# Performance work log

Hardware: AMD Instinct MI355X
Metric: run time of the kernel (lower is better)

The kernel has to match this reference:

```python
import jax, jax.numpy as jnp
import numpy as np

B, S = 16, 1024
V, D, P = 100000, 256, 8


def setup_inputs() -> dict:
    key = jax.random.key(0)
    k1, k2, k3, k4 = jax.random.split(key, 4)
    x = jax.random.randint(k1, (B, S), 0, V, dtype=jnp.int64 if jax.config.jax_enable_x64 else jnp.int32)
    emb_table = jax.random.normal(k2, (V, D), dtype=jnp.float32)
    weight = jax.random.normal(k3, (P, D, D), dtype=jnp.float32)
    partitions = jax.random.randint(k4, (V,), 0, P, dtype=jnp.int32)
    return {"x": x, "emb_table": emb_table, "weight": weight, "partitions": partitions}


def reference(x, emb_table, weight, partitions):
    P_, Dz, Dx = weight.shape
    # mask[p, x] = 1 for x < D >> p (reset_parameters halves active dim per partition)
    active = (Dx >> jnp.arange(P_))  # [P]
    mask = (jnp.arange(Dx)[None, :] < active[:, None]).astype(weight.dtype)  # [P, Dx]
    mw = weight * mask[:, None, :]  # [P, Dz, Dx], masked partition weights

    emb = emb_table[x]          # [B, S, Dx] token embeddings
    part = partitions[x]        # [B, S] partition id per token

    # Compute all P candidate outputs (small fixed P), then select per token.
    # Mathematically identical to gathering mw[part] and doing per-token matvec,
    # but avoids the huge [B,S,Dz,Dx] gathered-weight intermediate.
    all_out = jnp.einsum('bsx,pzx->bspz', emb, mw)  # [B, S, P, Dz]
    out = jnp.take_along_axis(all_out, part[..., None, None], axis=2)[..., 0, :]  # [B, S, Dz]
    return out
```

## Files before the change

### kernel.cpp

```cpp
#include <hip/hip_runtime.h>

__global__ void bucket_k(const int* __restrict__ x, const int* __restrict__ parts,
                         int* __restrict__ counts, int* __restrict__ buckets, int NT) {
    __shared__ int lcount[8];
    __shared__ int lbase[8];
    const int tid = threadIdx.x;
    if (tid < 8) lcount[tid] = 0;
    __syncthreads();

    const int i = blockIdx.x * blockDim.x + tid;
    int p = 0, lpos = 0;
    const bool valid = (i < NT);
    if (valid) {
        p = parts[x[i]];
        lpos = atomicAdd(&lcount[p], 1);
    }
    __syncthreads();
    if (tid < 8)
        lbase[tid] = lcount[tid] ? atomicAdd(&counts[tid], lcount[tid]) : 0;
    __syncthreads();
    if (valid)
        buckets[(size_t)p * NT + lbase[p] + lpos] = i;
}

#define TT 32
#define KC 32
#define XB 80

__global__ __launch_bounds__(256)
void fge_gemm(const int* __restrict__ x,
              const float* __restrict__ emb,
              const float* __restrict__ weight,
              const int* __restrict__ counts,
              const int* __restrict__ buckets,
              float* __restrict__ out, int NT) {
    const int p = blockIdx.y;
    const int n = counts[p];
    if ((int)(blockIdx.x * TT) >= n) return;
    const int K   = 256 >> p;
    const int nch = (K + KC - 1) / KC;
    const int tid = threadIdx.x;

    __shared__ __align__(16) float e_lds[KC][TT];
    __shared__ __align__(16) float w_lds[KC][256];
    __shared__ int vrow[TT];
    __shared__ int oidx[TT];

    const int tt  = tid & 7;
    const int tz  = tid >> 3;
    const int t_s = tid & 31;
    const int xh  = tid >> 5;

    for (int t0 = blockIdx.x * TT; t0 < n; t0 += XB * TT) {
        const int ntile = min(TT, n - t0);

        __syncthreads();
        if (tid < TT) {
            int idx = 0, row = 0;
            if (tid < ntile) {
                idx = buckets[(size_t)p * NT + t0 + tid];
                row = x[idx];
            }
            oidx[tid] = idx;
            vrow[tid] = row;
        }
        __syncthreads();

        float acc[4][8] = {};

        for (int ch = 0; ch < nch; ++ch) {
            {
                const bool tv = (t_s < ntile);
                const int gxb = ch * KC + xh * 4;
                const float4 v = *(const float4*)(emb + (size_t)vrow[t_s] * 256 + gxb);
                const float va[4] = {v.x, v.y, v.z, v.w};
#pragma unroll
                for (int c = 0; c < 4; ++c)
                    e_lds[xh * 4 + c][t_s] = (tv && (gxb + c) < K) ? va[c] : 0.f;
            }
            {
                const float* wr = weight + ((size_t)p * 256 + tid) * 256 + ch * KC;
#pragma unroll
                for (int i = 0; i < KC / 4; ++i) {
                    const float4 v = *(const float4*)(wr + i * 4);
                    w_lds[i * 4 + 0][tid] = v.x;
                    w_lds[i * 4 + 1][tid] = v.y;
                    w_lds[i * 4 + 2][tid] = v.z;
                    w_lds[i * 4 + 3][tid] = v.w;
                }
            }
            __syncthreads();

#pragma unroll
            for (int c = 0; c < KC; ++c) {
                const float4 ev = *(const float4*)&e_lds[c][tt * 4];
                const float4 w0 = *(const float4*)&w_lds[c][tz * 8];
                const float4 w1 = *(const float4*)&w_lds[c][tz * 8 + 4];
                const float ea[4] = {ev.x, ev.y, ev.z, ev.w};
                const float wa[8] = {w0.x, w0.y, w0.z, w0.w, w1.x, w1.y, w1.z, w1.w};
#pragma unroll
                for (int i = 0; i < 4; ++i)
#pragma unroll
                    for (int j = 0; j < 8; ++j)
                        acc[i][j] = fmaf(ea[i], wa[j], acc[i][j]);
            }
            __syncthreads();
        }

#pragma unroll
        for (int i = 0; i < 4; ++i) {
            const int t = tt * 4 + i;
            if (t < ntile) {
                float* op = out + (size_t)oidx[t] * 256 + tz * 8;
                float4 o0 = {acc[i][0], acc[i][1], acc[i][2], acc[i][3]};
                float4 o1 = {acc[i][4], acc[i][5], acc[i][6], acc[i][7]};
                *(float4*)op = o0;
                *(float4*)(op + 4) = o1;
            }
        }
    }
}

__global__ void naive_k(const int* __restrict__ x, const float* __restrict__ emb,
                        const float* __restrict__ w, const int* __restrict__ parts,
                        float* __restrict__ out, int D, int P) {
    const int i = blockIdx.x;
    const int tokrow = x[i];
    const int p = parts[tokrow];
    const int K = D >> p;
    const float* er = emb + (size_t)tokrow * D;
    for (int z = threadIdx.x; z < D; z += blockDim.x) {
        const float* wr = w + ((size_t)p * D + z) * D;
        float acc = 0.f;
        for (int k = 0; k < K; ++k) acc = fmaf(er[k], wr[k], acc);
        out[(size_t)i * D + z] = acc;
    }
}

extern "C" void kernel_launch(void* const* d_in, const int* in_sizes, int n_in,
                              void* d_out, int out_size, void* d_ws, size_t ws_size,
                              hipStream_t stream) {
    const int*   xi    = (const int*)d_in[0];
    const float* emb   = (const float*)d_in[1];
    const float* wgt   = (const float*)d_in[2];
    const int*   parts = (const int*)d_in[3];
    float* out = (float*)d_out;

    const int NT = in_sizes[0];
    const long long V = in_sizes[3];
    const int D = (int)(in_sizes[1] / V);
    const int P = (int)(in_sizes[2] / ((long long)D * D));
    const size_t need = 32 + (size_t)P * (size_t)NT * sizeof(int);

    if (D == 256 && P == 8 && ws_size >= need) {
        int* counts  = (int*)d_ws;
        int* buckets = (int*)((char*)d_ws + 32);
        hipMemsetAsync(counts, 0, 32, stream);
        bucket_k<<<(NT + 255) / 256, 256, 0, stream>>>(xi, parts, counts, buckets, NT);
        dim3 grid(XB, 8);
        fge_gemm<<<grid, 256, 0, stream>>>(xi, emb, wgt, counts, buckets, out, NT);
    } else {
        naive_k<<<NT, 256, 0, stream>>>(xi, emb, wgt, parts, out, D, P);
    }
}
```

Baseline: 170.0 us.

## Retile bucketed GEMM into 64-token by 64-output tiles with swizzled LDS

Reorganizes the per-partition GEMM to split the output dimension across 4 blocks (a new grid z dimension for partitions) with 64-token tiles. Each thread now computes 4 tokens by 4 outputs. The K chunk adapts to the partition's active width, up to 64, with a minimum of 16, so small partitions waste less padding. Weight LDS is stored transposed with an XOR-like rotation to avoid bank conflicts. The aim is more parallel blocks, better coalesced embedding loads and less wasted work on masked K, at the cost of re-gathering embeddings for each of the 4 z-blocks.

```diff
diff --git a/kernel.cpp b/kernel.cpp
--- a/kernel.cpp
+++ b/kernel.cpp
@@ -23,9 +23,8 @@
         buckets[(size_t)p * NT + lbase[p] + lpos] = i;
 }
 
-#define TT 32
-#define KC 32
-#define XB 80
+#define TT 64
+#define XB 40
 
 __global__ __launch_bounds__(256)
 void fge_gemm(const int* __restrict__ x,
@@ -34,22 +33,23 @@
               const int* __restrict__ counts,
               const int* __restrict__ buckets,
               float* __restrict__ out, int NT) {
-    const int p = blockIdx.y;
+    const int p = blockIdx.z;
     const int n = counts[p];
     if ((int)(blockIdx.x * TT) >= n) return;
+    const int z0  = blockIdx.y * 64;
     const int K   = 256 >> p;
-    const int nch = (K + KC - 1) / KC;
+    const int KP  = (K < 16) ? 16 : K;
+    const int KC  = (KP < 64) ? KP : 64;
+    const int nch = KP / KC;
     const int tid = threadIdx.x;
 
-    __shared__ __align__(16) float e_lds[KC][TT];
-    __shared__ __align__(16) float w_lds[KC][256];
+    __shared__ __align__(16) float e_lds[TT * 64];
+    __shared__ __align__(16) float w_lds[64 * 64];
     __shared__ int vrow[TT];
     __shared__ int oidx[TT];
 
-    const int tt  = tid & 7;
-    const int tz  = tid >> 3;
-    const int t_s = tid & 31;
-    const int xh  = tid >> 5;
+    const int tg  = tid >> 4;
+    const int zg4 = (tid & 15) * 4;
 
     for (int t0 = blockIdx.x * TT; t0 < n; t0 += XB * TT) {
         const int ntile = min(TT, n - t0);
@@ -66,56 +66,82 @@
         }
         __syncthreads();
 
-        float acc[4][8] = {};
+        float acc[4][4] = {};
 
         for (int ch = 0; ch < nch; ++ch) {
+            const int kbase = ch * KC;
+            const int lpr   = KC >> 2;
+
             {
-                const bool tv = (t_s < ntile);
-                const int gxb = ch * KC + xh * 4;
-                const float4 v = *(const float4*)(emb + (size_t)vrow[t_s] * 256 + gxb);
-                const float va[4] = {v.x, v.y, v.z, v.w};
-#pragma unroll
-                for (int c = 0; c < 4; ++c)
-                    e_lds[xh * 4 + c][t_s] = (tv && (gxb + c) < K) ? va[c] : 0.f;
+                const int passes = (TT * lpr) >> 8;
+                for (int ps = 0; ps < passes; ++ps) {
+                    const int idx = ps * 256 + tid;
+                    const int row = idx / lpr;
+                    const int c4  = (idx - row * lpr) * 4;
+                    const float4 v = *(const float4*)(emb + (size_t)vrow[row] * 256 + kbase + c4);
+                    float4 o;
+                    o.x = (kbase + c4 + 0 < K) ? v.x : 0.f;
+                    o.y = (kbase + c4 + 1 < K) ? v.y : 0.f;
+                    o.z = (kbase + c4 + 2 < K) ? v.z : 0.f;
+                    o.w = (kbase + c4 + 3 < K) ? v.w : 0.f;
+                    *(float4*)&e_lds[row * KC + c4] = o;
+                }
             }
             {
-                const float* wr = weight + ((size_t)p * 256 + tid) * 256 + ch * KC;
+                const int passes = (64 * lpr) >> 8;
+                for (int ps = 0; ps < passes; ++ps) {
+                    const int idx = ps * 256 + tid;
+                    const int rz  = idx / lpr;
+                    const int c4  = (idx - rz * lpr) * 4;
+                    const float4 v = *(const float4*)(weight + ((size_t)p * 256 + z0 + rz) * 256 + kbase + c4);
+                    const float vv[4] = {v.x, v.y, v.z, v.w};
 #pragma unroll
-                for (int i = 0; i < KC / 4; ++i) {
-                    const float4 v = *(const float4*)(wr + i * 4);
-                    w_lds[i * 4 + 0][tid] = v.x;
-                    w_lds[i * 4 + 1][tid] = v.y;
-                    w_lds[i * 4 + 2][tid] = v.z;
-                    w_lds[i * 4 + 3][tid] = v.w;
+                    for (int j = 0; j < 4; ++j) {
+                        const int kk = c4 + j;
+                        w_lds[kk * 64 + ((rz + 4 * kk) & 63)] =
+                            (kbase + kk < K) ? vv[j] : 0.f;
+                    }
                 }
             }
             __syncthreads();
 
+            const float* e0 = &e_lds[(tg * 4 + 0) * KC];
+            const float* e1 = &e_lds[(tg * 4 + 1) * KC];
+            const float* e2 = &e_lds[(tg * 4 + 2) * KC];
+            const float* e3 = &e_lds[(tg * 4 + 3) * KC];
+#pragma unroll 2
+            for (int k = 0; k < KC; k += 4) {
+                const float4 a0 = *(const float4*)(e0 + k);
+                const float4 a1 = *(const float4*)(e1 + k);
+                const float4 a2 = *(const float4*)(e2 + k);
+                const float4 a3 = *(const float4*)(e3 + k);
+                float4 w[4];
 #pragma unroll
-            for (int c = 0; c < KC; ++c) {
-                const float4 ev = *(const float4*)&e_lds[c][tt * 4];
-                const float4 w0 = *(const float4*)&w_lds[c][tz * 8];
-                const float4 w1 = *(const float4*)&w_lds[c][tz * 8 + 4];
-                const float ea[4] = {ev.x, ev.y, ev.z, ev.w};
-                const float wa[8] = {w0.x, w0.y, w0.z, w0.w, w1.x, w1.y, w1.z, w1.w};
+                for (int j = 0; j < 4; ++j)
+                    w[j] = *(const float4*)&w_lds[(k + j) * 64 + ((zg4 + 4 * (k + j)) & 63)];
+                const float ea[4][4] = {{a0.x,a0.y,a0.z,a0.w}, {a1.x,a1.y,a1.z,a1.w},
+                                        {a2.x,a2.y,a2.z,a2.w}, {a3.x,a3.y,a3.z,a3.w}};
+                const float wv[4][4] = {{w[0].x,w[0].y,w[0].z,w[0].w}, {w[1].x,w[1].y,w[1].z,w[1].w},
+                                        {w[2].x,w[2].y,w[2].z,w[2].w}, {w[3].x,w[3].y,w[3].z,w[3].w}};
 #pragma unroll
                 for (int i = 0; i < 4; ++i)
 #pragma unroll
-                    for (int j = 0; j < 8; ++j)
-                        acc[i][j] = fmaf(ea[i], wa[j], acc[i][j]);
+                    for (int j = 0; j < 4; ++j) {
+                        acc[i][0] = fmaf(ea[i][j], wv[j][0], acc[i][0]);
+                        acc[i][1] = fmaf(ea[i][j], wv[j][1], acc[i][1]);
+                        acc[i][2] = fmaf(ea[i][j], wv[j][2], acc[i][2]);
+                        acc[i][3] = fmaf(ea[i][j], wv[j][3], acc[i][3]);
+                    }
             }
             __syncthreads();
         }
 
 #pragma unroll
         for (int i = 0; i < 4; ++i) {
-            const int t = tt * 4 + i;
+            const int t = tg * 4 + i;
             if (t < ntile) {
-                float* op = out + (size_t)oidx[t] * 256 + tz * 8;
-                float4 o0 = {acc[i][0], acc[i][1], acc[i][2], acc[i][3]};
-                float4 o1 = {acc[i][4], acc[i][5], acc[i][6], acc[i][7]};
-                *(float4*)op = o0;
-                *(float4*)(op + 4) = o1;
+                float4 o = {acc[i][0], acc[i][1], acc[i][2], acc[i][3]};
+                *(float4*)(out + (size_t)oidx[t] * 256 + z0 + zg4) = o;
             }
         }
     }
@@ -157,7 +183,7 @@
         int* buckets = (int*)((char*)d_ws + 32);
         hipMemsetAsync(counts, 0, 32, stream);
         bucket_k<<<(NT + 255) / 256, 256, 0, stream>>>(xi, parts, counts, buckets, NT);
-        dim3 grid(XB, 8);
+        dim3 grid(XB, 4, 8);
         fge_gemm<<<grid, 256, 0, stream>>>(xi, emb, wgt, counts, buckets, out, NT);
     } else {
         naive_k<<<NT, 256, 0, stream>>>(xi, emb, wgt, parts, out, D, P);
```

Measured after the change: 168.0 us. No clear change (-1.2%).

## Replace FP32 FMA tile GEMM with bf16 MFMA matrix-core kernel

Applied to the files above, without the earlier changes.

Replaces the scalar FP32 register-tiled GEMM with a kernel built on the 16x16x32 bf16 MFMA instruction. Weights and gathered embeddings are converted to bf16 as they are staged into padded LDS tiles. Token tiles grow to 64 and the K chunk adapts to the partition's active width. This targets the FP32 ALU-bound inner loop, but lowers input precision to bf16, which may affect accuracy tolerance. Weights are still converted again on every tile.

```diff
diff --git a/kernel.cpp b/kernel.cpp
--- a/kernel.cpp
+++ b/kernel.cpp
@@ -1,4 +1,14 @@
 #include <hip/hip_runtime.h>
+
+typedef unsigned short u16;
+typedef unsigned int   u32;
+typedef __attribute__((ext_vector_type(8))) __bf16 bf16x8;
+typedef __attribute__((ext_vector_type(4))) float  f32x4;
+
+__device__ __forceinline__ u16 f2bf(float f) {
+    u32 u = __float_as_uint(f);
+    return (u16)((u + 0x7FFFu + ((u >> 16) & 1u)) >> 16);
+}
 
 __global__ void bucket_k(const int* __restrict__ x, const int* __restrict__ parts,
                          int* __restrict__ counts, int* __restrict__ buckets, int NT) {
@@ -7,7 +17,6 @@
     const int tid = threadIdx.x;
     if (tid < 8) lcount[tid] = 0;
     __syncthreads();
-
     const int i = blockIdx.x * blockDim.x + tid;
     int p = 0, lpos = 0;
     const bool valid = (i < NT);
@@ -23,12 +32,12 @@
         buckets[(size_t)p * NT + lbase[p] + lpos] = i;
 }
 
-#define TT 32
-#define KC 32
-#define XB 80
+#define TT 64
+#define XB 40
+#define SJ 72
 
 __global__ __launch_bounds__(256)
-void fge_gemm(const int* __restrict__ x,
+void fge_mfma(const int* __restrict__ x,
               const float* __restrict__ emb,
               const float* __restrict__ weight,
               const int* __restrict__ counts,
@@ -38,22 +47,23 @@
     const int n = counts[p];
     if ((int)(blockIdx.x * TT) >= n) return;
     const int K   = 256 >> p;
+    const int KC  = (K >= 64) ? 64 : 32;
     const int nch = (K + KC - 1) / KC;
-    const int tid = threadIdx.x;
+    const int shf = (KC == 64) ? 4 : 3;
+    const int lpr = 1 << shf;
+    const int tid  = threadIdx.x;
+    const int lane = tid & 63;
+    const int wv   = tid >> 6;
+    const int l15  = lane & 15;
+    const int lq   = lane >> 4;
 
-    __shared__ __align__(16) float e_lds[KC][TT];
-    __shared__ __align__(16) float w_lds[KC][256];
+    __shared__ u16 w_lds[256 * SJ];
+    __shared__ u16 e_lds[TT * SJ];
     __shared__ int vrow[TT];
     __shared__ int oidx[TT];
 
-    const int tt  = tid & 7;
-    const int tz  = tid >> 3;
-    const int t_s = tid & 31;
-    const int xh  = tid >> 5;
-
     for (int t0 = blockIdx.x * TT; t0 < n; t0 += XB * TT) {
         const int ntile = min(TT, n - t0);
-
         __syncthreads();
         if (tid < TT) {
             int idx = 0, row = 0;
@@ -66,56 +76,71 @@
         }
         __syncthreads();
 
-        float acc[4][8] = {};
+        f32x4 acc[4][4];
+#pragma unroll
+        for (int mi = 0; mi < 4; ++mi)
+#pragma unroll
+            for (int ni = 0; ni < 4; ++ni)
+                acc[mi][ni] = (f32x4){0.f, 0.f, 0.f, 0.f};
 
         for (int ch = 0; ch < nch; ++ch) {
-            {
-                const bool tv = (t_s < ntile);
-                const int gxb = ch * KC + xh * 4;
-                const float4 v = *(const float4*)(emb + (size_t)vrow[t_s] * 256 + gxb);
-                const float va[4] = {v.x, v.y, v.z, v.w};
-#pragma unroll
-                for (int c = 0; c < 4; ++c)
-                    e_lds[xh * 4 + c][t_s] = (tv && (gxb + c) < K) ? va[c] : 0.f;
+            const int kb = ch * KC;
+
+            for (int idx = tid; idx < (256 << shf); idx += 256) {
+                const int rz = idx >> shf;
+                const int c4 = (idx & (lpr - 1)) * 4;
+                const float4 v = *(const float4*)(weight + ((size_t)p * 256 + rz) * 256 + kb + c4);
+                ushort4 h;
+                h.x = (kb + c4 + 0 < K) ? f2bf(v.x) : (u16)0;
+                h.y = (kb + c4 + 1 < K) ? f2bf(v.y) : (u16)0;
+                h.z = (kb + c4 + 2 < K) ? f2bf(v.z) : (u16)0;
+                h.w = (kb + c4 + 3 < K) ? f2bf(v.w) : (u16)0;
+                *(ushort4*)&w_lds[rz * SJ + c4] = h;
             }
-            {
-                const float* wr = weight + ((size_t)p * 256 + tid) * 256 + ch * KC;
-#pragma unroll
-                for (int i = 0; i < KC / 4; ++i) {
-                    const float4 v = *(const float4*)(wr + i * 4);
-                    w_lds[i * 4 + 0][tid] = v.x;
-                    w_lds[i * 4 + 1][tid] = v.y;
-                    w_lds[i * 4 + 2][tid] = v.z;
-                    w_lds[i * 4 + 3][tid] = v.w;
-                }
+            for (int idx = tid; idx < (TT << shf); idx += 256) {
+                const int rt = idx >> shf;
+                const int c4 = (idx & (lpr - 1)) * 4;
+                const float4 v = *(const float4*)(emb + (size_t)vrow[rt] * 256 + kb + c4);
+                ushort4 h;
+                h.x = (kb + c4 + 0 < K) ? f2bf(v.x) : (u16)0;
+                h.y = (kb + c4 + 1 < K) ? f2bf(v.y) : (u16)0;
+                h.z = (kb + c4 + 2 < K) ? f2bf(v.z) : (u16)0;
+                h.w = (kb + c4 + 3 < K) ? f2bf(v.w) : (u16)0;
+                *(ushort4*)&e_lds[rt * SJ + c4] = h;
             }
             __syncthreads();
 
+            const int ksteps = KC >> 5;
+            for (int ks = 0; ks < ksteps; ++ks) {
+                const int ko = ks * 32 + lq * 8;
+                bf16x8 a[4], b[4];
 #pragma unroll
-            for (int c = 0; c < KC; ++c) {
-                const float4 ev = *(const float4*)&e_lds[c][tt * 4];
-                const float4 w0 = *(const float4*)&w_lds[c][tz * 8];
-                const float4 w1 = *(const float4*)&w_lds[c][tz * 8 + 4];
-                const float ea[4] = {ev.x, ev.y, ev.z, ev.w};
-                const float wa[8] = {w0.x, w0.y, w0.z, w0.w, w1.x, w1.y, w1.z, w1.w};
+                for (int mi = 0; mi < 4; ++mi)
+                    a[mi] = *(const bf16x8*)&w_lds[(wv * 64 + mi * 16 + l15) * SJ + ko];
 #pragma unroll
-                for (int i = 0; i < 4; ++i)
+                for (int ni = 0; ni < 4; ++ni)
+                    b[ni] = *(const bf16x8*)&e_lds[(ni * 16 + l15) * SJ + ko];
 #pragma unroll
-                    for (int j = 0; j < 8; ++j)
-                        acc[i][j] = fmaf(ea[i], wa[j], acc[i][j]);
+                for (int mi = 0; mi < 4; ++mi)
+#pragma unroll
+                    for (int ni = 0; ni < 4; ++ni)
+                        acc[mi][ni] = __builtin_amdgcn_mfma_f32_16x16x32_bf16(
+                            a[mi], b[ni], acc[mi][ni], 0, 0, 0);
             }
             __syncthreads();
         }
 
 #pragma unroll
-        for (int i = 0; i < 4; ++i) {
-            const int t = tt * 4 + i;
+        for (int ni = 0; ni < 4; ++ni) {
+            const int t = ni * 16 + l15;
             if (t < ntile) {
-                float* op = out + (size_t)oidx[t] * 256 + tz * 8;
-                float4 o0 = {acc[i][0], acc[i][1], acc[i][2], acc[i][3]};
-                float4 o1 = {acc[i][4], acc[i][5], acc[i][6], acc[i][7]};
-                *(float4*)op = o0;
-                *(float4*)(op + 4) = o1;
+                float* ob = out + (size_t)oidx[t] * 256;
+#pragma unroll
+                for (int mi = 0; mi < 4; ++mi) {
+                    const int z = wv * 64 + mi * 16 + lq * 4;
+                    float4 o = {acc[mi][ni].x, acc[mi][ni].y, acc[mi][ni].z, acc[mi][ni].w};
+                    *(float4*)(ob + z) = o;
+                }
             }
         }
     }
@@ -158,7 +183,7 @@
         hipMemsetAsync(counts, 0, 32, stream);
         bucket_k<<<(NT + 255) / 256, 256, 0, stream>>>(xi, parts, counts, buckets, NT);
         dim3 grid(XB, 8);
-        fge_gemm<<<grid, 256, 0, stream>>>(xi, emb, wgt, counts, buckets, out, NT);
+        fge_mfma<<<grid, 256, 0, stream>>>(xi, emb, wgt, counts, buckets, out, NT);
     } else {
         naive_k<<<NT, 256, 0, stream>>>(xi, emb, wgt, parts, out, D, P);
     }
```

Result: slower. 185.7 us (+9.2%).
